# Optimization experiments

Measured on AMD Instinct MI355X. Metric: run time of the kernel, lower is better.

Reference implementation:

```python
import jax, jax.numpy as jnp
import numpy as np

B, M, LSEQ, D, K, H, DFF, NL = 16, 512, 1024, 128, 16, 8, 512, 2


def layernorm(x, g, b):
    mu = x.mean(-1, keepdims=True)
    var = ((x - mu) ** 2).mean(-1, keepdims=True)
    return (x - mu) * jax.lax.rsqrt(var + 1e-5) * g + b


def gcn_conv(x, row, col, W, b, N):
    # PyG GCNConv: xW, add self-loops, symmetric D^-1/2 (A+I) D^-1/2 aggregation
    xw = x @ W
    loop = jnp.arange(N)
    row2 = jnp.concatenate([row, loop])
    col2 = jnp.concatenate([col, loop])
    deg = jax.ops.segment_sum(jnp.ones(row2.shape[0], xw.dtype), col2, num_segments=N)
    dinv = jnp.where(deg > 0, jax.lax.rsqrt(deg), 0.0)
    norm = dinv[row2] * dinv[col2]  # [E+N]
    out = jax.ops.segment_sum(norm[:, None] * xw[row2], col2, num_segments=N)
    return out + b


def encoder_layer(q, kv, Wq, Wk, Wv, Wo, ln1_g, ln1_b, W1, b1, W2, b2, ln2_g, ln2_b):
    Bb, Mq, d = q.shape
    dh = d // H
    qh = (q @ Wq).reshape(Bb, Mq, H, dh)
    kh = (kv @ Wk).reshape(Bb, -1, H, dh)
    vh = (kv @ Wv).reshape(Bb, -1, H, dh)
    scores = jnp.einsum('bqhd,bkhd->bhqk', qh, kh) / jnp.sqrt(jnp.float32(dh))
    attn = jax.nn.softmax(scores, axis=-1)
    o = jnp.einsum('bhqk,bkhd->bqhd', attn, vh).reshape(Bb, Mq, d) @ Wo
    x = layernorm(q + o, ln1_g, ln1_b)
    ff = jax.nn.relu(x @ W1 + b1) @ W2 + b2
    return layernorm(x + ff, ln2_g, ln2_b)


def setup_inputs() -> dict:
    key = jax.random.key(0)
    ks = jax.random.split(key, 24)
    s = 0.05
    return {
        'enc_out_vari': jax.random.normal(ks[0], (B, M, D), jnp.float32),
        'x_enc': jax.random.normal(ks[1], (B, LSEQ, M), jnp.float32),
        'gcn_w1': jax.random.normal(ks[2], (D, D), jnp.float32) * s,
        'gcn_b1': jnp.zeros((D,), jnp.float32),
        'gcn_w2': jax.random.normal(ks[3], (D, D), jnp.float32) * s,
        'gcn_b2': jnp.zeros((D,), jnp.float32),
        'Wq': jax.random.normal(ks[4], (NL, D, D), jnp.float32) * s,
        'Wk': jax.random.normal(ks[5], (NL, D, D), jnp.float32) * s,
        'Wv': jax.random.normal(ks[6], (NL, D, D), jnp.float32) * s,
        'Wo': jax.random.normal(ks[7], (NL, D, D), jnp.float32) * s,
        'ln1_g': jnp.ones((NL, D), jnp.float32),
        'ln1_b': jnp.zeros((NL, D), jnp.float32),
        'W1': jax.random.normal(ks[8], (NL, D, DFF), jnp.float32) * s,
        'b1': jnp.zeros((NL, DFF), jnp.float32),
        'W2': jax.random.normal(ks[9], (NL, DFF, D), jnp.float32) * s,
        'b2': jnp.zeros((NL, D), jnp.float32),
        'ln2_g': jnp.ones((NL, D), jnp.float32),
        'ln2_b': jnp.zeros((NL, D), jnp.float32),
    }


def reference(enc_out_vari, x_enc, gcn_w1, gcn_b1, gcn_w2, gcn_b2, Wq, Wk, Wv, Wo,
              ln1_g, ln1_b, W1, b1, W2, b2, ln2_g, ln2_b):
    Bb, Mm, d = enc_out_vari.shape
    # --- Pearson correlation kNN graph build (ascending argsort as in source) ---
    xt = x_enc.transpose(0, 2, 1)  # [B, M, L]
    c = xt - xt.mean(-1, keepdims=True)
    cov = jnp.einsum('bml,bnl->bmn', c, c) / jnp.float32(LSEQ - 1)
    std = jnp.sqrt(jnp.diagonal(cov, axis1=-2, axis2=-1))
    std = jnp.where(std == 0, 1.0, std)
    corr = cov / (std[:, :, None] * std[:, None, :])
    neighbors = jnp.argsort(corr, axis=-1)[:, :, 1:K + 1]  # [B, M, K]
    # rows tiled, cols node-major (faithful to source's repeat/reshape mismatch)
    row = jnp.tile(jnp.arange(Mm), K)[None, :]           # [1, M*K]
    col = neighbors.reshape(Bb, -1)                      # [B, M*K]
    offs = (jnp.arange(Bb) * Mm)[:, None]
    row_g = jnp.broadcast_to(row + offs, (Bb, Mm * K)).reshape(-1)
    col_g = (col + offs).reshape(-1)
    N = Bb * Mm
    # --- 2-layer GCN on the disjoint-union graph (dropout is identity in eval) ---
    x_raw = enc_out_vari.reshape(N, d)
    x1 = jax.nn.relu(gcn_conv(x_raw, row_g, col_g, gcn_w1, gcn_b1, N))
    x2 = jax.nn.relu(gcn_conv(x1, row_g, col_g, gcn_w2, gcn_b2, N))
    kv = x2.reshape(Bb, Mm, d)
    # --- Transformer encoder: enc_out_vari attends to GCN features ---
    h = enc_out_vari
    for l in range(NL):
        h = encoder_layer(h, kv, Wq[l], Wk[l], Wv[l], Wo[l], ln1_g[l], ln1_b[l],
                          W1[l], b1[l], W2[l], b2[l], ln2_g[l], ln2_b[l])
    return h
```

## Files before the change

kernel.cpp:

```cpp
#include <hip/hip_runtime.h>
#include <math.h>

#define BB 16
#define MM 512
#define LL 1024
#define DD 128
#define KK 16
#define HH 8
#define DHH 16
#define NDFF 512
#define NNODE (BB*MM)
#define NEDGE (NNODE*KK)

typedef __attribute__((ext_vector_type(8))) short bf16x8;
typedef __attribute__((ext_vector_type(4))) float f32x4;
#define MFMA(a,b,c) __builtin_amdgcn_mfma_f32_16x16x32_bf16(a,b,c,0,0,0)

__device__ inline unsigned short bf16rne(float x) {
  union { float f; unsigned u; } v; v.f = x;
  return (unsigned short)((v.u + 0x7FFFu + ((v.u >> 16) & 1u)) >> 16);
}
__device__ inline float bf16tof(unsigned short h) {
  union { unsigned u; float f; } v; v.u = ((unsigned)h) << 16; return v.f;
}
__device__ inline void hilo(float x, unsigned short& h, unsigned short& l) {
  h = bf16rne(x);
  l = bf16rne(x - bf16tof(h));
}

__device__ inline void async16(const void* g, void* l) {
  __builtin_amdgcn_global_load_lds(
      (const __attribute__((address_space(1))) unsigned int*)g,
      (__attribute__((address_space(3))) unsigned int*)l, 16, 0, 0);
}

__global__ __launch_bounds__(256) void transpose_x_kernel(const float* __restrict__ X,
                                                          unsigned short* __restrict__ XTh,
                                                          unsigned short* __restrict__ XTl) {
  __shared__ float t[32][33];
  int b = blockIdx.z;
  int m0 = blockIdx.x * 32, l0 = blockIdx.y * 32;
  int c = threadIdx.x & 31, r = threadIdx.x >> 5;
  const float* Xb = X + (size_t)b * LL * MM;
  #pragma unroll
  for (int i = 0; i < 4; ++i)
    t[r + i*8][c] = Xb[(size_t)(l0 + r + i*8) * MM + m0 + c];
  __syncthreads();
  int R = m0 >> 6;
  int rbase = m0 & 63;
  size_t base = ((size_t)(b * 8 + R)) * 65536 + (size_t)(l0 >> 5) * 2048
              + (size_t)(c >> 3) * 512 + (c & 7);
  #pragma unroll
  for (int i = 0; i < 4; ++i) {
    unsigned short h, l;
    hilo(t[c][r + i*8], h, l);
    size_t idx = base + (size_t)(rbase + r + i*8) * 8;
    XTh[idx] = h; XTl[idx] = l;
  }
}

__global__ __launch_bounds__(256) void transpose_w_kernel(
    const float* __restrict__ gw1, const float* __restrict__ gw2,
    const float* __restrict__ Wq, const float* __restrict__ Wk,
    const float* __restrict__ Wv, const float* __restrict__ Wo,
    const float* __restrict__ W1, const float* __restrict__ W2,
    unsigned short* __restrict__ wTh, unsigned short* __restrict__ wTl) {
  int z = blockIdx.z;
  const float* src; int K, N; size_t doff;
  if (z < 10) {
    K = 128; N = 128;
    switch (z) {
      case 0: src = gw1;         doff = 0;         break;
      case 1: src = gw2;         doff = 16384;     break;
      case 2: src = Wk;          doff = 2*16384;   break;
      case 3: src = Wv;          doff = 3*16384;   break;
      case 4: src = Wk + 16384;  doff = 4*16384;   break;
      case 5: src = Wv + 16384;  doff = 5*16384;   break;
      case 6: src = Wq;          doff = 6*16384;   break;
      case 7: src = Wq + 16384;  doff = 7*16384;   break;
      case 8: src = Wo;          doff = 8*16384;   break;
      default: src = Wo + 16384; doff = 9*16384;   break;
    }
  } else if (z < 12) {
    K = 128; N = 512; doff = 163840 + (size_t)(z - 10) * 65536;
    src = W1 + (size_t)(z - 10) * 65536;
  } else {
    K = 512; N = 128; doff = 294912 + (size_t)(z - 12) * 65536;
    src = W2 + (size_t)(z - 12) * 65536;
  }
  int k0 = blockIdx.x * 32, n0 = blockIdx.y * 32;
  if (k0 >= K || n0 >= N) return;
  __shared__ float t[32][33];
  int c = threadIdx.x & 31, r = threadIdx.x >> 5;
  #pragma unroll
  for (int i = 0; i < 4; ++i)
    t[r + i*8][c] = src[(size_t)(k0 + r + i*8) * N + n0 + c];
  __syncthreads();
  #pragma unroll
  for (int i = 0; i < 4; ++i) {
    size_t idx = doff + (size_t)(n0 + r + i*8) * K + k0 + c;
    unsigned short h, l;
    hilo(t[c][r + i*8], h, l);
    wTh[idx] = h; wTl[idx] = l;
  }
}

__global__ void split_kernel(const float* __restrict__ in,
                             unsigned short* __restrict__ h,
                             unsigned short* __restrict__ l) {
  int i = blockIdx.x * 256 + threadIdx.x;
  float4 v = ((const float4*)in)[i];
  unsigned short h0,h1,h2,h3,l0,l1,l2,l3;
  hilo(v.x,h0,l0); hilo(v.y,h1,l1); hilo(v.z,h2,l2); hilo(v.w,h3,l3);
  uint2 hh, ll;
  hh.x = (unsigned)h0 | ((unsigned)h1 << 16); hh.y = (unsigned)h2 | ((unsigned)h3 << 16);
  ll.x = (unsigned)l0 | ((unsigned)l1 << 16); ll.y = (unsigned)l2 | ((unsigned)l3 << 16);
  ((uint2*)h)[i] = hh; ((uint2*)l)[i] = ll;
}

__global__ void colmean_part_kernel(const float* __restrict__ X, float* __restrict__ part) {
  int bm = blockIdx.x * 256 + threadIdx.x;
  int b = bm >> 9, m = bm & (MM - 1);
  int l0 = blockIdx.y * 128;
  const float* p = X + (size_t)b * LL * MM + (size_t)l0 * MM + m;
  float s = 0.f;
  #pragma unroll 8
  for (int l = 0; l < 128; ++l) s += p[(size_t)l * MM];
  part[(size_t)blockIdx.y * NNODE + bm] = s;
}

__global__ void colmean_finish_kernel(const float* __restrict__ part, float* __restrict__ mu) {
  int bm = blockIdx.x * 256 + threadIdx.x;
  float s = 0.f;
  #pragma unroll
  for (int j = 0; j < 8; ++j) s += part[(size_t)j * NNODE + bm];
  mu[bm] = s * (1.f / 1024.f);
}

__global__ __launch_bounds__(256) void gram_kernel(const unsigned short* __restrict__ XTh,
                                                   const unsigned short* __restrict__ XTl,
                                                   float* __restrict__ G0,
                                                   float* __restrict__ G1) {
  __shared__ unsigned short lAh[2048], lAl[2048], lBh[2048], lBl[2048];
  int b = blockIdx.y, z = blockIdx.z;
  int pi = blockIdx.x;
  int ti = 0, rem = pi;
  while (rem >= 8 - ti) { rem -= 8 - ti; ++ti; }
  int tj = ti + rem;
  int tid = threadIdx.x;
  int wid = tid >> 6, lane = tid & 63;
  int wr = wid >> 1, wc = wid & 1;
  int fr = lane & 15, fkb = lane >> 4;
  size_t abase = ((size_t)(b * 8 + ti)) * 65536 + (size_t)z * 16 * 2048;
  size_t bbase = ((size_t)(b * 8 + tj)) * 65536 + (size_t)z * 16 * 2048;
  int toff = tid * 8;
  int aoff0 = fkb * 512 + (wr*32 + fr) * 8;
  int aoff1 = aoff0 + 128;
  int boff0 = fkb * 512 + (wc*32 + fr) * 8;
  int boff1 = boff0 + 128;
  f32x4 acc00 = {0,0,0,0}, acc01 = {0,0,0,0}, acc10 = {0,0,0,0}, acc11 = {0,0,0,0};
  for (int s = 0; s < 16; ++s) {
    size_t ao = abase + (size_t)s * 2048 + toff;
    size_t bo = bbase + (size_t)s * 2048 + toff;
    async16(XTh + ao, lAh + toff);
    async16(XTl + ao, lAl + toff);
    async16(XTh + bo, lBh + toff);
    async16(XTl + bo, lBl + toff);
    __syncthreads();
    bf16x8 a0h = *(const bf16x8*)(lAh + aoff0);
    bf16x8 a1h = *(const bf16x8*)(lAh + aoff1);
    bf16x8 a0l = *(const bf16x8*)(lAl + aoff0);
    bf16x8 a1l = *(const bf16x8*)(lAl + aoff1);
    bf16x8 b0h = *(const bf16x8*)(lBh + boff0);
    bf16x8 b1h = *(const bf16x8*)(lBh + boff1);
    bf16x8 b0l = *(const bf16x8*)(lBl + boff0);
    bf16x8 b1l = *(const bf16x8*)(lBl + boff1);
    acc00 = MFMA(a0h, b0h, acc00); acc00 = MFMA(a0h, b0l, acc00); acc00 = MFMA(a0l, b0h, acc00);
    acc01 = MFMA(a0h, b1h, acc01); acc01 = MFMA(a0h, b1l, acc01); acc01 = MFMA(a0l, b1h, acc01);
    acc10 = MFMA(a1h, b0h, acc10); acc10 = MFMA(a1h, b0l, acc10); acc10 = MFMA(a1l, b0h, acc10);
    acc11 = MFMA(a1h, b1h, acc11); acc11 = MFMA(a1h, b1l, acc11); acc11 = MFMA(a1l, b1h, acc11);
    __syncthreads();
  }
  int m0 = ti * 64, n0 = tj * 64;
  float* G = (z ? G1 : G0) + (size_t)b * MM * MM;
  int mirror = (ti != tj);
  #pragma unroll
  for (int i = 0; i < 2; ++i) {
    #pragma unroll
    for (int j = 0; j < 2; ++j) {
      const f32x4& a = (i == 0) ? (j == 0 ? acc00 : acc01) : (j == 0 ? acc10 : acc11);
      #pragma unroll
      for (int r = 0; r < 4; ++r) {
        int row = m0 + wr*32 + i*16 + (lane >> 4)*4 + r;
        int col = n0 + wc*32 + j*16 + (lane & 15);
        float v = a[r];
        G[(size_t)row * MM + col] = v;
        if (mirror) G[(size_t)col * MM + row] = v;
      }
    }
  }
}

__global__ __launch_bounds__(256) void bf_gemm_k128_kernel(
    const unsigned short* __restrict__ Ah, const unsigned short* __restrict__ Al,
    const unsigned short* __restrict__ Bh, const unsigned short* __restrict__ Bl,
    float* __restrict__ C, unsigned short* __restrict__ Ch, unsigned short* __restrict__ Cl,
    int Ldc, int col0, const float* __restrict__ bias,
    const float* __restrict__ resid, int relu) {
  int tid = threadIdx.x;
  int m0 = blockIdx.y * 64, n0 = blockIdx.x * 64;
  int wid = tid >> 6, lane = tid & 63;
  int wr = wid >> 1, wc = wid & 1;
  int fr = lane & 15, fkb = lane >> 4;
  size_t arow0 = (size_t)(m0 + wr*32 + fr) * 128;
  size_t arow1 = arow0 + 16 * 128;
  size_t brow0 = (size_t)(n0 + wc*32 + fr) * 128;
  size_t brow1 = brow0 + 16 * 128;
  bf16x8 fa0h[4], fa1h[4], fa0l[4], fa1l[4];
  bf16x8 fb0h[4], fb1h[4], fb0l[4], fb1l[4];
  #pragma unroll
  for (int ks = 0; ks < 4; ++ks) {
    int ko = ks * 32 + fkb * 8;
    fa0h[ks] = *(const bf16x8*)(Ah + arow0 + ko);
    fa1h[ks] = *(const bf16x8*)(Ah + arow1 + ko);
    fa0l[ks] = *(const bf16x8*)(Al + arow0 + ko);
    fa1l[ks] = *(const bf16x8*)(Al + arow1 + ko);
    fb0h[ks] = *(const bf16x8*)(Bh + brow0 + ko);
    fb1h[ks] = *(const bf16x8*)(Bh + brow1 + ko);
    fb0l[ks] = *(const bf16x8*)(Bl + brow0 + ko);
    fb1l[ks] = *(const bf16x8*)(Bl + brow1 + ko);
  }
  f32x4 acc00 = {0,0,0,0}, acc01 = {0,0,0,0}, acc10 = {0,0,0,0}, acc11 = {0,0,0,0};
  #pragma unroll
  for (int ks = 0; ks < 4; ++ks) {
    acc00 = MFMA(fa0h[ks], fb0h[ks], acc00);
    acc00 = MFMA(fa0h[ks], fb0l[ks], acc00);
    acc00 = MFMA(fa0l[ks], fb0h[ks], acc00);
    acc01 = MFMA(fa0h[ks], fb1h[ks], acc01);
    acc01 = MFMA(fa0h[ks], fb1l[ks], acc01);
    acc01 = MFMA(fa0l[ks], fb1h[ks], acc01);
    acc10 = MFMA(fa1h[ks], fb0h[ks], acc10);
    acc10 = MFMA(fa1h[ks], fb0l[ks], acc10);
    acc10 = MFMA(fa1l[ks], fb0h[ks], acc10);
    acc11 = MFMA(fa1h[ks], fb1h[ks], acc11);
    acc11 = MFMA(fa1h[ks], fb1l[ks], acc11);
    acc11 = MFMA(fa1l[ks], fb1h[ks], acc11);
  }
  #pragma unroll
  for (int i = 0; i < 2; ++i) {
    #pragma unroll
    for (int j = 0; j < 2; ++j) {
      const f32x4& a = (i == 0) ? (j == 0 ? acc00 : acc01) : (j == 0 ? acc10 : acc11);
      #pragma unroll
      for (int r = 0; r < 4; ++r) {
        int row = m0 + wr*32 + i*16 + (lane >> 4)*4 + r;
        int col = col0 + n0 + wc*32 + j*16 + (lane & 15);
        float v = a[r];
        if (bias)  v += bias[col - col0];
        if (resid) v += resid[(size_t)row * Ldc + col];
        if (relu)  v = fmaxf(v, 0.f);
        size_t o = (size_t)row * Ldc + col;
        if (C) C[o] = v;
        if (Ch) {
          if (Cl) {
            unsigned short hh, ll;
            hilo(v, hh, ll);
            Ch[o] = hh; Cl[o] = ll;
          } else {
            Ch[o] = bf16rne(v);
          }
        }
      }
    }
  }
}

__global__ __launch_bounds__(512) void bf_gemm_sk_kernel(
    const unsigned short* __restrict__ Ah, const unsigned short* __restrict__ Al,
    const unsigned short* __restrict__ Bh, const unsigned short* __restrict__ Bl,
    float* __restrict__ C, unsigned short* __restrict__ Ch, unsigned short* __restrict__ Cl,
    int Ldc, int col0, int Kd, const float* __restrict__ bias,
    const float* __restrict__ resid, int relu) {
  __shared__ float red[64][65];
  int tid = threadIdx.x;
  int m0 = blockIdx.y * 64, n0 = blockIdx.x * 64;
  int wid = tid >> 6, lane = tid & 63;
  int kg = wid >> 2;
  int w4 = wid & 3;
  int wr = w4 >> 1, wc = w4 & 1;
  int fr = lane & 15, fkb = lane >> 4;
  int Kh = Kd >> 1;
  size_t arow0 = (size_t)(m0 + wr*32 + fr) * Kd + (size_t)kg * Kh;
  size_t arow1 = arow0 + (size_t)16 * Kd;
  size_t brow0 = (size_t)(n0 + wc*32 + fr) * Kd + (size_t)kg * Kh;
  size_t brow1 = brow0 + (size_t)16 * Kd;
  f32x4 acc00 = {0,0,0,0}, acc01 = {0,0,0,0}, acc10 = {0,0,0,0}, acc11 = {0,0,0,0};
  int ko = fkb * 8;
  bf16x8 a0h = *(const bf16x8*)(Ah + arow0 + ko);
  bf16x8 a1h = *(const bf16x8*)(Ah + arow1 + ko);
  bf16x8 a0l = *(const bf16x8*)(Al + arow0 + ko);
  bf16x8 a1l = *(const bf16x8*)(Al + arow1 + ko);
  bf16x8 b0h = *(const bf16x8*)(Bh + brow0 + ko);
  bf16x8 b1h = *(const bf16x8*)(Bh + brow1 + ko);
  bf16x8 b0l = *(const bf16x8*)(Bl + brow0 + ko);
  bf16x8 b1l = *(const bf16x8*)(Bl + brow1 + ko);
  for (int k0 = 32; k0 < Kh; k0 += 32) {
    int kn = k0 + fkb * 8;
    bf16x8 na0h = *(const bf16x8*)(Ah + arow0 + kn);
    bf16x8 na1h = *(const bf16x8*)(Ah + arow1 + kn);
    bf16x8 na0l = *(const bf16x8*)(Al + arow0 + kn);
    bf16x8 na1l = *(const bf16x8*)(Al + arow1 + kn);
    bf16x8 nb0h = *(const bf16x8*)(Bh + brow0 + kn);
    bf16x8 nb1h = *(const bf16x8*)(Bh + brow1 + kn);
    bf16x8 nb0l = *(const bf16x8*)(Bl + brow0 + kn);
    bf16x8 nb1l = *(const bf16x8*)(Bl + brow1 + kn);
    acc00 = MFMA(a0h, b0h, acc00); acc00 = MFMA(a0h, b0l, acc00); acc00 = MFMA(a0l, b0h, acc00);
    acc01 = MFMA(a0h, b1h, acc01); acc01 = MFMA(a0h, b1l, acc01); acc01 = MFMA(a0l, b1h, acc01);
    acc10 = MFMA(a1h, b0h, acc10); acc10 = MFMA(a1h, b0l, acc10); acc10 = MFMA(a1l, b0h, acc10);
    acc11 = MFMA(a1h, b1h, acc11); acc11 = MFMA(a1h, b1l, acc11); acc11 = MFMA(a1l, b1h, acc11);
    a0h = na0h; a1h = na1h; a0l = na0l; a1l = na1l;
    b0h = nb0h; b1h = nb1h; b0l = nb0l; b1l = nb1l;
  }
  acc00 = MFMA(a0h, b0h, acc00); acc00 = MFMA(a0h, b0l, acc00); acc00 = MFMA(a0l, b0h, acc00);
  acc01 = MFMA(a0h, b1h, acc01); acc01 = MFMA(a0h, b1l, acc01); acc01 = MFMA(a0l, b1h, acc01);
  acc10 = MFMA(a1h, b0h, acc10); acc10 = MFMA(a1h, b0l, acc10); acc10 = MFMA(a1l, b0h, acc10);
  acc11 = MFMA(a1h, b1h, acc11); acc11 = MFMA(a1h, b1l, acc11); acc11 = MFMA(a1l, b1h, acc11);
  if (kg == 1) {
    #pragma unroll
    for (int i = 0; i < 2; ++i) {
      #pragma unroll
      for (int j = 0; j < 2; ++j) {
        const f32x4& a = (i == 0) ? (j == 0 ? acc00 : acc01) : (j == 0 ? acc10 : acc11);
        #pragma unroll
        for (int r = 0; r < 4; ++r) {
          int lr = wr*32 + i*16 + (lane >> 4)*4 + r;
          int lc = wc*32 + j*16 + (lane & 15);
          red[lr][lc] = a[r];
        }
      }
    }
  }
  __syncthreads();
  if (kg == 0) {
    #pragma unroll
    for (int i = 0; i < 2; ++i) {
      #pragma unroll
      for (int j = 0; j < 2; ++j) {
        const f32x4& a = (i == 0) ? (j == 0 ? acc00 : acc01) : (j == 0 ? acc10 : acc11);
        #pragma unroll
        for (int r = 0; r < 4; ++r) {
          int lr = wr*32 + i*16 + (lane >> 4)*4 + r;
          int lc = wc*32 + j*16 + (lane & 15);
          int row = m0 + lr;
          int col = col0 + n0 + lc;
          float v = a[r] + red[lr][lc];
          if (bias)  v += bias[col - col0];
          if (resid) v += resid[(size_t)row * Ldc + col];
          if (relu)  v = fmaxf(v, 0.f);
          size_t o = (size_t)row * Ldc + col;
          if (C) C[o] = v;
          if (Ch) {
            unsigned short hh, ll;
            hilo(v, hh, ll);
            Ch[o] = hh; Cl[o] = ll;
          }
        }
      }
    }
  }
}

__global__ void rstd_kernel(const float* __restrict__ G0, const float* __restrict__ G1,
                            const float* __restrict__ mu, float* __restrict__ rstd) {
  int bm = blockIdx.x * 256 + threadIdx.x;
  int b = bm >> 9, m = bm & (MM - 1);
  size_t di = (size_t)b * MM * MM + (size_t)m * MM + m;
  float g = G0[di] + G1[di];
  float mm = mu[bm];
  float cov = (g - 1024.f * mm * mm) * (1.f / 1023.f);
  float sd = sqrtf(fmaxf(cov, 0.f));
  rstd[bm] = (sd == 0.f) ? 1.f : (1.f / sd);
}

__global__ void select_kernel(const float* __restrict__ G0, const float* __restrict__ G1,
                              const float* __restrict__ mu,
                              const float* __restrict__ rstd, int* __restrict__ nb) {
  int w = threadIdx.x >> 6, lane = threadIdx.x & 63;
  int bm = blockIdx.x * 4 + w;
  int b = bm >> 9, m = bm & (MM - 1);
  size_t rowoff = (size_t)b * MM * MM + (size_t)m * MM;
  const float* Gr0 = G0 + rowoff;
  const float* Gr1 = G1 + rowoff;
  const float* mub = mu + b * MM;
  const float* rsb = rstd + b * MM;
  float mm = mub[m], rm = rsb[m];
  float vals[8];
  int excl = 0;
  #pragma unroll
  for (int j = 0; j < 8; ++j) {
    int n = lane + j * 64;
    float cov = ((Gr0[n] + Gr1[n]) - 1024.f * mm * mub[n]) * (1.f / 1023.f);
    vals[j] = cov * rm * rsb[n];
  }
  int* out = nb + (size_t)bm * KK;
  for (int it = 0; it < KK + 1; ++it) {
    float bv = 1e30f; int bi = 1 << 30;
    #pragma unroll
    for (int j = 0; j < 8; ++j) {
      if (!((excl >> j) & 1)) {
        int n = lane + j * 64;
        if (vals[j] < bv) { bv = vals[j]; bi = n; }
      }
    }
    for (int off = 32; off; off >>= 1) {
      float v2 = __shfl_down(bv, off);
      int   i2 = __shfl_down(bi, off);
      if (v2 < bv || (v2 == bv && i2 < bi)) { bv = v2; bi = i2; }
    }
    bi = __shfl(bi, 0);
    if ((bi & 63) == lane) excl |= 1 << (bi >> 6);
    if (it > 0 && lane == 0) out[it - 1] = bi;
  }
}

__global__ void count_kernel(const int* __restrict__ nb, int* __restrict__ cnt) {
  int e = blockIdx.x * 256 + threadIdx.x;
  int b = e >> 13, i = e & 8191;
  int dst = b * MM + nb[(size_t)b * 8192 + i];
  atomicAdd(&cnt[dst], 1);
}

__global__ void scan_kernel(const int* __restrict__ cnt, int* __restrict__ offs,
                            int* __restrict__ curs, float* __restrict__ dinv) {
  __shared__ int part[256];
  int tid = threadIdx.x;
  int base = tid * 32;
  int local[32];
  int s = 0;
  #pragma unroll
  for (int i = 0; i < 32; ++i) { local[i] = cnt[base + i]; s += local[i]; }
  part[tid] = s;
  __syncthreads();
  for (int off = 1; off < 256; off <<= 1) {
    int v = (tid >= off) ? part[tid - off] : 0;
    __syncthreads();
    part[tid] += v;
    __syncthreads();
  }
  int run = part[tid] - s;
  #pragma unroll
  for (int i = 0; i < 32; ++i) {
    int n = base + i;
    offs[n] = run; curs[n] = run;
    run += local[i];
    dinv[n] = rsqrtf((float)(local[i] + 1));
  }
  if (tid == 255) offs[NNODE] = run;
}

__global__ void scatter_kernel(const int* __restrict__ nb, int* __restrict__ curs,
                               int* __restrict__ lists) {
  int e = blockIdx.x * 256 + threadIdx.x;
  int b = e >> 13, i = e & 8191;
  int dst = b * MM + nb[(size_t)b * 8192 + i];
  int src = b * MM + (i & (MM - 1));
  int pos = atomicAdd(&curs[dst], 1);
  lists[pos] = src;
}

__global__ void agg_kernel(const float* __restrict__ xw, const float* __restrict__ dinv,
                           const int* __restrict__ offs, const int* __restrict__ lists,
                           const float* __restrict__ bias,
                           unsigned short* __restrict__ outh,
                           unsigned short* __restrict__ outl) {
  int n = blockIdx.x * 2 + (threadIdx.x >> 7);
  int c = threadIdx.x & 127;
  float dn = dinv[n];
  float s = dn * xw[(size_t)n * DD + c];
  int e0 = offs[n], e1 = offs[n + 1];
  for (int e = e0; e < e1; ++e) {
    int src = lists[e];
    s += dinv[src] * xw[(size_t)src * DD + c];
  }
  float v = fmaxf(dn * s + bias[c], 0.f);
  unsigned short hh, ll;
  hilo(v, hh, ll);
  size_t o = (size_t)n * DD + c;
  outh[o] = hh; outl[o] = ll;
}

__global__ __launch_bounds__(256) void attn_mfma_kernel(
    const unsigned short* __restrict__ Qb16, const unsigned short* __restrict__ KV16,
    int kvoff,
    unsigned short* __restrict__ outh, unsigned short* __restrict__ outl) {
  __shared__ unsigned short Kl[512 * 16];
  __shared__ unsigned short VT[16 * 520];
  __shared__ unsigned short Pl[64 * 136];
  int bx = blockIdx.x;
  int qc = bx & 7;
  int h  = (bx >> 3) & 7;
  int b  = bx >> 6;
  int tid = threadIdx.x;

  for (int u = tid; u < 1024; u += 256) {
    int row = u >> 1, half = u & 1;
    const unsigned short* src = KV16 + (size_t)(b * MM + row) * 512 + kvoff + h * 16 + half * 8;
    *(uint4*)&Kl[row * 16 + half * 8] = *(const uint4*)src;
  }
  for (int key = tid; key < 512; key += 256) {
    const unsigned short* src = KV16 + (size_t)(b * MM + key) * 512 + kvoff + 128 + h * 16;
    unsigned short tmp[16];
    *(uint4*)&tmp[0] = *(const uint4*)src;
    *(uint4*)&tmp[8] = *(const uint4*)(src + 8);
    #pragma unroll
    for (int d = 0; d < 16; ++d) VT[d * 520 + key] = tmp[d];
  }
  __syncthreads();

  int wid = tid >> 6, lane = tid & 63;
  int lq = lane & 15, g = lane >> 4;
  bf16x8 zz = {0,0,0,0,0,0,0,0};
  bf16x8 qf = zz;
  if (lane < 32) {
    int qrow = b * MM + qc * 64 + wid * 16 + lq;
    qf = *(const bf16x8*)(Qb16 + (size_t)qrow * 128 + h * 16 + g * 8);
  }
  float m = -1e30f, lp = 0.f;
  f32x4 o = {0,0,0,0};
  int prow = (wid * 16 + lq) * 136;

  for (int c4 = 0; c4 < 4; ++c4) {
    int kbase = c4 * 128;
    f32x4 s[8];
    f32x4 zc = {0,0,0,0};
    #pragma unroll
    for (int t = 0; t < 8; ++t) {
      bf16x8 kf = zz;
      if (lane < 32) kf = *(const bf16x8*)&Kl[(kbase + t * 16 + lq) * 16 + g * 8];
      s[t] = MFMA(kf, qf, zc);
    }
    float tm = -1e30f;
    #pragma unroll
    for (int t = 0; t < 8; ++t) {
      tm = fmaxf(tm, fmaxf(fmaxf(s[t][0], s[t][1]), fmaxf(s[t][2], s[t][3])));
    }
    tm = fmaxf(tm, __shfl_xor(tm, 16));
    tm = fmaxf(tm, __shfl_xor(tm, 32));
    float nm = fmaxf(m, 0.25f * tm);
    float esc = __expf(m - nm);
    m = nm;
    float ls = 0.f;
    #pragma unroll
    for (int t = 0; t < 8; ++t) {
      float p0 = __expf(0.25f * s[t][0] - nm);
      float p1 = __expf(0.25f * s[t][1] - nm);
      float p2 = __expf(0.25f * s[t][2] - nm);
      float p3 = __expf(0.25f * s[t][3] - nm);
      ls += (p0 + p1) + (p2 + p3);
      unsigned w0 = (unsigned)bf16rne(p0) | ((unsigned)bf16rne(p1) << 16);
      unsigned w1 = (unsigned)bf16rne(p2) | ((unsigned)bf16rne(p3) << 16);
      int kc = t * 16 + g * 4;
      *(unsigned*)&Pl[prow + kc]     = w0;
      *(unsigned*)&Pl[prow + kc + 2] = w1;
    }
    lp = lp * esc + ls;
    float e0 = __shfl(esc, g * 4 + 0);
    float e1 = __shfl(esc, g * 4 + 1);
    float e2 = __shfl(esc, g * 4 + 2);
    float e3 = __shfl(esc, g * 4 + 3);
    o[0] *= e0; o[1] *= e1; o[2] *= e2; o[3] *= e3;
    #pragma unroll
    for (int c = 0; c < 4; ++c) {
      bf16x8 pf = *(const bf16x8*)&Pl[prow + c * 32 + g * 8];
      bf16x8 vf = *(const bf16x8*)&VT[lq * 520 + kbase + c * 32 + g * 8];
      o = MFMA(pf, vf, o);
    }
  }
  lp += __shfl_xor(lp, 16);
  lp += __shfl_xor(lp, 32);
  float linv = 1.f / lp;
  float l0 = __shfl(linv, g * 4 + 0);
  float l1 = __shfl(linv, g * 4 + 1);
  float l2 = __shfl(linv, g * 4 + 2);
  float l3 = __shfl(linv, g * 4 + 3);
  float vv[4] = {o[0] * l0, o[1] * l1, o[2] * l2, o[3] * l3};
  #pragma unroll
  for (int r = 0; r < 4; ++r) {
    int qrow = b * MM + qc * 64 + wid * 16 + g * 4 + r;
    size_t off = (size_t)qrow * DD + h * 16 + lq;
    unsigned short hh, ll;
    hilo(vv[r], hh, ll);
    outh[off] = hh; outl[off] = ll;
  }
}

__global__ void ln_kernel(const float* __restrict__ x, const float* __restrict__ g,
                          const float* __restrict__ bb, float* __restrict__ out,
                          unsigned short* __restrict__ outh,
                          unsigned short* __restrict__ outl) {
  int row = blockIdx.x * 4 + (threadIdx.x >> 6);
  int lane = threadIdx.x & 63;
  float2 xv = *(const float2*)&x[(size_t)row * DD + lane * 2];
  float s = xv.x + xv.y;
  #pragma unroll
  for (int off = 1; off < 64; off <<= 1) s += __shfl_xor(s, off);
  float mu = s * (1.f / 128.f);
  float d0 = xv.x - mu, d1 = xv.y - mu;
  float sq = d0 * d0 + d1 * d1;
  #pragma unroll
  for (int off = 1; off < 64; off <<= 1) sq += __shfl_xor(sq, off);
  float rs = rsqrtf(sq * (1.f / 128.f) + 1e-5f);
  float2 gg = *(const float2*)&g[lane * 2];
  float2 bv = *(const float2*)&bb[lane * 2];
  float2 y;
  y.x = d0 * rs * gg.x + bv.x;
  y.y = d1 * rs * gg.y + bv.y;
  *(float2*)&out[(size_t)row * DD + lane * 2] = y;
  if (outh) {
    unsigned short h0, l0, h1, l1;
    hilo(y.x, h0, l0); hilo(y.y, h1, l1);
    unsigned hh = (unsigned)h0 | ((unsigned)h1 << 16);
    unsigned ll = (unsigned)l0 | ((unsigned)l1 << 16);
    *(unsigned*)&outh[(size_t)row * DD + lane * 2] = hh;
    *(unsigned*)&outl[(size_t)row * DD + lane * 2] = ll;
  }
}

extern "C" void kernel_launch(void* const* d_in, const int* in_sizes, int n_in,
                              void* d_out, int out_size, void* d_ws, size_t ws_size,
                              hipStream_t stream) {
  (void)in_sizes; (void)n_in; (void)out_size; (void)ws_size;
  const float* enc  = (const float*)d_in[0];
  const float* xenc = (const float*)d_in[1];
  const float* gw1  = (const float*)d_in[2];
  const float* gb1  = (const float*)d_in[3];
  const float* gw2  = (const float*)d_in[4];
  const float* gb2  = (const float*)d_in[5];
  const float* Wq   = (const float*)d_in[6];
  const float* Wk   = (const float*)d_in[7];
  const float* Wv   = (const float*)d_in[8];
  const float* Wo   = (const float*)d_in[9];
  const float* ln1g = (const float*)d_in[10];
  const float* ln1b = (const float*)d_in[11];
  const float* W1   = (const float*)d_in[12];
  const float* b1   = (const float*)d_in[13];
  const float* W2   = (const float*)d_in[14];
  const float* b2   = (const float*)d_in[15];
  const float* ln2g = (const float*)d_in[16];
  const float* ln2b = (const float*)d_in[17];
  float* outp = (float*)d_out;

  char* w = (char*)d_ws;
  auto alloc = [&](size_t bytes) -> char* {
    char* p = w;
    w += (bytes + 255) & ~(size_t)255;
    return p;
  };
  float* mu    = (float*)alloc((size_t)NNODE * 4);
  float* rstd  = (float*)alloc((size_t)NNODE * 4);
  float* dinv  = (float*)alloc((size_t)NNODE * 4);
  float* mpart = (float*)alloc((size_t)8 * NNODE * 4);
  int*   nb    = (int*)  alloc((size_t)NEDGE * 4);
  int*   cnt   = (int*)  alloc((size_t)NNODE * 4);
  int*   offs  = (int*)  alloc((size_t)(NNODE + 1) * 4);
  int*   curs  = (int*)  alloc((size_t)NNODE * 4);
  int*   lists = (int*)  alloc((size_t)NEDGE * 4);
  float* gram  = (float*)alloc((size_t)BB * MM * MM * 4);
  float* gram2 = (float*)alloc((size_t)BB * MM * MM * 4);
  float* bufx  = (float*)alloc((size_t)NNODE * DD * 4);
  float* bufxl = (float*)alloc((size_t)NNODE * DD * 4);
  float* bufh  = (float*)alloc((size_t)NNODE * DD * 4);
  float* bufh1 = (float*)alloc((size_t)NNODE * DD * 4);
  unsigned short* xth  = (unsigned short*)alloc((size_t)BB * MM * LL * 2);
  unsigned short* xtl  = (unsigned short*)alloc((size_t)BB * MM * LL * 2);
  unsigned short* wTh  = (unsigned short*)alloc((size_t)425984 * 2);
  unsigned short* wTl  = (unsigned short*)alloc((size_t)425984 * 2);
  unsigned short* ench = (unsigned short*)alloc((size_t)NNODE * DD * 2);
  unsigned short* encl = (unsigned short*)alloc((size_t)NNODE * DD * 2);
  unsigned short* x1h  = (unsigned short*)alloc((size_t)NNODE * DD * 2);
  unsigned short* x1l  = (unsigned short*)alloc((size_t)NNODE * DD * 2);
  unsigned short* kvbh = (unsigned short*)alloc((size_t)NNODE * DD * 2);
  unsigned short* kvbl = (unsigned short*)alloc((size_t)NNODE * DD * 2);
  unsigned short* xlh  = (unsigned short*)alloc((size_t)NNODE * DD * 2);
  unsigned short* xll  = (unsigned short*)alloc((size_t)NNODE * DD * 2);
  unsigned short* h1h  = (unsigned short*)alloc((size_t)NNODE * DD * 2);
  unsigned short* h1l  = (unsigned short*)alloc((size_t)NNODE * DD * 2);
  unsigned short* sdh  = (unsigned short*)alloc((size_t)NNODE * DD * 2);
  unsigned short* sdl  = (unsigned short*)alloc((size_t)NNODE * DD * 2);

  unsigned short* Qb16 = (unsigned short*)gram;
  unsigned short* KV16 = (unsigned short*)(gram + (size_t)1048576);
  unsigned short* ffh = (unsigned short*)gram2;
  unsigned short* ffl = (unsigned short*)gram2 + (size_t)NNODE * NDFF;

  const unsigned short* gw1Th = wTh,         *gw1Tl = wTl;
  const unsigned short* gw2Th = wTh + 16384, *gw2Tl = wTl + 16384;
  const unsigned short* KVTh01 = wTh + (size_t)2 * 16384;
  const unsigned short* KVTl01 = wTl + (size_t)2 * 16384;
  auto WqTh = [&](int l) { return wTh + (size_t)(6 + l) * 16384; };
  auto WqTl = [&](int l) { return wTl + (size_t)(6 + l) * 16384; };
  auto WoTh = [&](int l) { return wTh + (size_t)(8 + l) * 16384; };
  auto WoTl = [&](int l) { return wTl + (size_t)(8 + l) * 16384; };
  auto W1Th = [&](int l) { return wTh + 163840 + (size_t)l * 65536; };
  auto W1Tl = [&](int l) { return wTl + 163840 + (size_t)l * 65536; };
  auto W2Th = [&](int l) { return wTh + 294912 + (size_t)l * 65536; };
  auto W2Tl = [&](int l) { return wTl + 294912 + (size_t)l * 65536; };

  auto gemm = [&](const unsigned short* Ah, const unsigned short* Al,
                  const unsigned short* Bh, const unsigned short* Bl,
                  float* C, unsigned short* Ch, unsigned short* Cl,
                  int Mr, int Ncols, int Ldc, int col0, int Kd,
                  const float* bias, const float* resid, int relu) {
    dim3 g(Ncols / 64, Mr / 64);
    if (Kd == 128) {
      bf_gemm_k128_kernel<<<g, 256, 0, stream>>>(Ah, Al, Bh, Bl, C, Ch, Cl, Ldc, col0,
                                                 bias, resid, relu);
    } else {
      bf_gemm_sk_kernel<<<g, 512, 0, stream>>>(Ah, Al, Bh, Bl, C, Ch, Cl, Ldc, col0, Kd,
                                               bias, resid, relu);
    }
  };

  transpose_x_kernel<<<dim3(16, 32, 16), 256, 0, stream>>>(xenc, xth, xtl);
  transpose_w_kernel<<<dim3(16, 16, 14), 256, 0, stream>>>(gw1, gw2, Wq, Wk, Wv, Wo, W1, W2, wTh, wTl);
  split_kernel<<<(NNODE * DD / 4) / 256, 256, 0, stream>>>(enc, ench, encl);

  colmean_part_kernel<<<dim3(32, 8), 256, 0, stream>>>(xenc, mpart);
  colmean_finish_kernel<<<NNODE / 256, 256, 0, stream>>>(mpart, mu);
  gram_kernel<<<dim3(36, BB, 2), 256, 0, stream>>>(xth, xtl, gram, gram2);
  rstd_kernel<<<NNODE / 256, 256, 0, stream>>>(gram, gram2, mu, rstd);
  select_kernel<<<NNODE / 4, 256, 0, stream>>>(gram, gram2, mu, rstd, nb);
  hipMemsetAsync(cnt, 0, (size_t)NNODE * 4, stream);
  count_kernel<<<NEDGE / 256, 256, 0, stream>>>(nb, cnt);
  scan_kernel<<<1, 256, 0, stream>>>(cnt, offs, curs, dinv);
  scatter_kernel<<<NEDGE / 256, 256, 0, stream>>>(nb, curs, lists);

  gemm(ench, encl, gw1Th, gw1Tl, bufx, nullptr, nullptr, NNODE, DD, DD, 0, DD,
       nullptr, nullptr, 0);
  agg_kernel<<<NNODE / 2, 256, 0, stream>>>(bufx, dinv, offs, lists, gb1, x1h, x1l);
  gemm(x1h, x1l, gw2Th, gw2Tl, bufx, nullptr, nullptr, NNODE, DD, DD, 0, DD,
       nullptr, nullptr, 0);
  agg_kernel<<<NNODE / 2, 256, 0, stream>>>(bufx, dinv, offs, lists, gb2, kvbh, kvbl);

  gemm(kvbh, kvbl, KVTh01, KVTl01, nullptr, KV16, nullptr, NNODE, 512, 512, 0, DD,
       nullptr, nullptr, 0);

  for (int l = 0; l < 2; ++l) {
    const float* hq = (l == 0) ? enc : bufh1;
    const unsigned short* hqh = (l == 0) ? ench : h1h;
    const unsigned short* hql = (l == 0) ? encl : h1l;
    gemm(hqh, hql, WqTh(l), WqTl(l), nullptr, Qb16, nullptr, NNODE, DD, DD, 0, DD,
         nullptr, nullptr, 0);
    attn_mfma_kernel<<<BB * HH * 8, 256, 0, stream>>>(Qb16, KV16, l * 256, sdh, sdl);
    gemm(sdh, sdl, WoTh(l), WoTl(l), bufx, nullptr, nullptr, NNODE, DD, DD, 0, DD,
         nullptr, hq, 0);
    ln_kernel<<<NNODE / 4, 256, 0, stream>>>(bufx, ln1g + l * DD, ln1b + l * DD, bufxl, xlh, xll);
    gemm(xlh, xll, W1Th(l), W1Tl(l), nullptr, ffh, ffl, NNODE, NDFF, NDFF, 0, DD,
         b1 + l * NDFF, nullptr, 1);
    gemm(ffh, ffl, W2Th(l), W2Tl(l), bufh, nullptr, nullptr, NNODE, DD, DD, 0, NDFF,
         b2 + l * DD, bufxl, 0);
    if (l == 1) {
      ln_kernel<<<NNODE / 4, 256, 0, stream>>>(bufh, ln2g + l * DD, ln2b + l * DD,
                                               outp, nullptr, nullptr);
    } else {
      ln_kernel<<<NNODE / 4, 256, 0, stream>>>(bufh, ln2g + l * DD, ln2b + l * DD,
                                               bufh1, h1h, h1l);
    }
  }
}
```

Measured before the change: 390.0 us.

## Extract top-17 neighbors via packed sort keys and two-at-a-time wave reduction

Top-K selection now packs each correlation value into an order-preserving 64-bit key with its index. Each lane sorts its 8 keys with a sorting network, and a butterfly shuffle reduction finds the two smallest keys per round. This takes 9 rounds instead of 17 sequential argmin reductions, cutting shuffle and reduction latency in the selection kernel. In exchange it adds 64-bit compares and shifting of the register list, and the select kernel is only one small part of the whole pipeline.

```diff
diff --git a/kernel.cpp b/kernel.cpp
--- a/kernel.cpp
+++ b/kernel.cpp
@@ -394,32 +394,72 @@
   const float* mub = mu + b * MM;
   const float* rsb = rstd + b * MM;
   float mm = mub[m], rm = rsb[m];
-  float vals[8];
-  int excl = 0;
+  unsigned long long k[8];
   #pragma unroll
   for (int j = 0; j < 8; ++j) {
     int n = lane + j * 64;
     float cov = ((Gr0[n] + Gr1[n]) - 1024.f * mm * mub[n]) * (1.f / 1023.f);
-    vals[j] = cov * rm * rsb[n];
-  }
+    float val = cov * rm * rsb[n];
+    union { float f; unsigned u; } cv; cv.f = val;
+    unsigned s = cv.u ^ ((unsigned)((int)cv.u >> 31) | 0x80000000u);
+    k[j] = ((unsigned long long)s << 32) | (unsigned)n;
+  }
+  #define CE(i, j) { unsigned long long lo = k[i] < k[j] ? k[i] : k[j]; \
+                     unsigned long long hi = k[i] < k[j] ? k[j] : k[i]; \
+                     k[i] = lo; k[j] = hi; }
+  CE(0,1) CE(2,3) CE(4,5) CE(6,7)
+  CE(0,2) CE(1,3) CE(4,6) CE(5,7)
+  CE(1,2) CE(5,6) CE(0,4) CE(3,7)
+  CE(1,5) CE(2,6)
+  CE(1,4) CE(3,6)
+  CE(2,4) CE(3,5)
+  CE(3,4)
+  #undef CE
+  const unsigned long long UMX = 0xFFFFFFFFFFFFFFFFull;
   int* out = nb + (size_t)bm * KK;
-  for (int it = 0; it < KK + 1; ++it) {
-    float bv = 1e30f; int bi = 1 << 30;
-    #pragma unroll
-    for (int j = 0; j < 8; ++j) {
-      if (!((excl >> j) & 1)) {
-        int n = lane + j * 64;
-        if (vals[j] < bv) { bv = vals[j]; bi = n; }
+  #pragma unroll 1
+  for (int r = 0; r < 9; ++r) {
+    unsigned long long c1 = k[0], c2 = k[1];
+    #pragma unroll
+    for (int lvl = 1; lvl <= 32; lvl <<= 1) {
+      unsigned long long o1 = __shfl_xor(c1, lvl);
+      unsigned long long o2 = __shfl_xor(c2, lvl);
+      unsigned long long lo = c1 < o1 ? c1 : o1;
+      unsigned long long hi = c1 < o1 ? o1 : c1;
+      unsigned long long m2 = c2 < o2 ? c2 : o2;
+      c1 = lo;
+      c2 = hi < m2 ? hi : m2;
+    }
+    if (lane == 0) {
+      if (r == 0) {
+        out[0] = (int)(unsigned)(c2 & 0xFFFFFFFFu);
+      } else if (r < 8) {
+        out[2*r - 1] = (int)(unsigned)(c1 & 0xFFFFFFFFu);
+        out[2*r]     = (int)(unsigned)(c2 & 0xFFFFFFFFu);
+      } else {
+        out[15] = (int)(unsigned)(c1 & 0xFFFFFFFFu);
       }
     }
-    for (int off = 32; off; off >>= 1) {
-      float v2 = __shfl_down(bv, off);
-      int   i2 = __shfl_down(bi, off);
-      if (v2 < bv || (v2 == bv && i2 < bi)) { bv = v2; bi = i2; }
-    }
-    bi = __shfl(bi, 0);
-    if ((bi & 63) == lane) excl |= 1 << (bi >> 6);
-    if (it > 0 && lane == 0) out[it - 1] = bi;
+    if (r < 8) {
+      bool hit = (k[0] == c1) || (k[0] == c2);
+      k[0] = hit ? k[1] : k[0];
+      k[1] = hit ? k[2] : k[1];
+      k[2] = hit ? k[3] : k[2];
+      k[3] = hit ? k[4] : k[3];
+      k[4] = hit ? k[5] : k[4];
+      k[5] = hit ? k[6] : k[5];
+      k[6] = hit ? k[7] : k[6];
+      k[7] = hit ? UMX  : k[7];
+      bool hit2 = (k[0] == c1) || (k[0] == c2);
+      k[0] = hit2 ? k[1] : k[0];
+      k[1] = hit2 ? k[2] : k[1];
+      k[2] = hit2 ? k[3] : k[2];
+      k[3] = hit2 ? k[4] : k[3];
+      k[4] = hit2 ? k[5] : k[4];
+      k[5] = hit2 ? k[6] : k[5];
+      k[6] = hit2 ? k[7] : k[6];
+      k[7] = hit2 ? UMX  : k[7];
+    }
   }
 }
 
```

Result: slower. 414.5 us (+6.3%).
